# Performance work log

Measured on AMD Instinct MI355X. Metric: run time of the kernel, lower is better.

## Reference

```python
import jax, jax.numpy as jnp
import numpy as np


def _edt_background(gt):
    """Exact Euclidean distance transform of (1 - gt): distance from each pixel
    to the nearest foreground (gt==1) pixel. gt: [H, W] int. Returns [H, W] f32.
    Separable formulation: g(i,j) = 1D distance along row i to nearest fg;
    D(i,j)^2 = min_{i'} ( (i-i')^2 + g(i',j)^2 ), which is the exact 2D EDT.
    """
    H, W = gt.shape
    BIG = jnp.float32(H + W)  # upper bound on any true distance
    fg = gt > 0
    col = jnp.arange(W, dtype=jnp.float32)
    # nearest fg index to the left (running max of fg column index)
    left = jax.lax.cummax(jnp.where(fg, col, -BIG), axis=1)
    d_left = col[None, :] - left
    # nearest fg index to the right: running max of (-col) from the right = -min(col)
    right = jax.lax.cummax(jnp.where(fg, -col, -BIG)[:, ::-1], axis=1)[:, ::-1]
    d_right = (-right) - col[None, :]
    g = jnp.clip(jnp.minimum(d_left, d_right), 0.0, BIG)  # [H, W] 1D row distances
    g2 = g * g
    row = jnp.arange(H, dtype=jnp.float32)
    di2 = (row[:, None] - row[None, :]) ** 2              # [H, H]
    d2 = jnp.min(di2[:, :, None] + g2[None, :, :], axis=1)  # [H, W]
    return jnp.sqrt(d2)


def setup_inputs() -> dict:
    key = jax.random.key(0)
    k1, k2 = jax.random.split(key)
    B, H, W = 16, 384, 384
    logits = jax.random.normal(k1, (B, 1, H, W), dtype=jnp.float32)
    targets = jax.random.randint(k2, (B, 1, H, W), 0, 2).astype(jnp.int32)
    return {"logits": logits, "targets": targets}


def reference(logits, targets):
    probs = jax.nn.sigmoid(logits)            # [B,1,H,W]
    gt = targets[:, 0]                        # [B,H,W] int
    # sequential map over batch keeps the [H,H,W] EDT intermediate per-sample
    dist = jax.lax.map(_edt_background, gt)   # [B,H,W] f32
    tgt_f = gt.astype(jnp.float32)
    per_sample = jnp.mean(jnp.abs(probs[:, 0] - tgt_f) * dist, axis=(1, 2))
    return jnp.mean(per_sample)
```

## Files before the change

### kernel.cpp

```cpp
#include <hip/hip_runtime.h>
#include <math.h>


#define BB 16
#define HH 384
#define WW 384
#define WPR 12
#define WPRP 13
#define SW 8
#define NBLK_PER_IMG (WW / SW)
#define THREADS 256
#define BIGD 768

__global__ __launch_bounds__(THREADS) void pack_kernel(
    const int* __restrict__ gt, unsigned* __restrict__ mask) {
  const int idx = blockIdx.x * THREADS + threadIdx.x;
  const bool fg = gt[idx] != 0;
  const unsigned long long m = __ballot(fg);
  const int lane = threadIdx.x & 63;
  if (lane == 0) mask[idx >> 5] = (unsigned)m;
  else if (lane == 32) mask[idx >> 5] = (unsigned)(m >> 32);
}

__global__ __launch_bounds__(THREADS) void boundary_loss_kernel(
    const float* __restrict__ logits, const int* __restrict__ targets,
    const unsigned* __restrict__ mask, float* __restrict__ out) {
  const int blk = blockIdx.x;
  const int b = blk / NBLK_PER_IMG;
  const int j0 = (blk % NBLK_PER_IMG) * SW;
  const int* __restrict__ gt = targets + b * HH * WW;
  const float* __restrict__ lg = logits + b * HH * WW;
  const unsigned* __restrict__ gm = mask + b * HH * WPR;

  __shared__ unsigned m_s[HH * WPRP];
  __shared__ unsigned short g_s[HH * SW];

  for (int s = threadIdx.x; s < HH * WPR; s += THREADS) {
    const int row = s / WPR;
    const int w = s - row * WPR;
    m_s[row * WPRP + w] = gm[s];
  }
  __syncthreads();

  for (int idx = threadIdx.x; idx < HH * SW; idx += THREADS) {
    const int i = idx >> 3;
    const int jj = idx & (SW - 1);
    const int j = j0 + jj;
    const unsigned* __restrict__ mr = m_s + i * WPRP;
    const int w = j >> 5, bpos = j & 31;
    const unsigned cur = mr[w];
    const unsigned lm = cur & (0xFFFFFFFFu >> (31 - bpos));
    int dl = BIGD;
    if (lm) {
      dl = bpos - (31 - __clz(lm));
    } else {
      for (int ww = w - 1; ww >= 0; --ww) {
        const unsigned x = mr[ww];
        if (x) { dl = j - (ww * 32 + 31 - __clz(x)); break; }
      }
    }
    const unsigned rm = cur & (0xFFFFFFFFu << bpos);
    int dr = BIGD;
    if (rm) {
      dr = (__ffs(rm) - 1) - bpos;
    } else {
      for (int ww = w + 1; ww < WPR; ++ww) {
        const unsigned x = mr[ww];
        if (x) { dr = ww * 32 + (__ffs(x) - 1) - j; break; }
      }
    }
    g_s[idx] = (unsigned short)min(min(dl, dr), BIGD);
  }
  __syncthreads();

  float acc = 0.0f;
  for (int idx = threadIdx.x; idx < HH * SW; idx += THREADS) {
    const int i = idx >> 3;
    const int jj = idx & (SW - 1);
    const int j = j0 + jj;
    const int g = g_s[idx];
    int best = g * g;
    for (int r = 1; r * r < best; ++r) {
      const int im = i - r, ip = i + r;
      if (im >= 0) { const int v = g_s[im * SW + jj]; best = min(best, r * r + v * v); }
      if (ip < HH) { const int v = g_s[ip * SW + jj]; best = min(best, r * r + v * v); }
    }
    const float dist = sqrtf((float)best);
    const float x = lg[i * WW + j];
    const float p = 1.0f / (1.0f + expf(-x));
    const float t = (float)gt[i * WW + j];
    acc += fabsf(p - t) * dist;
  }

  __shared__ float red[THREADS / 64];
  for (int off = 32; off > 0; off >>= 1) acc += __shfl_down(acc, off, 64);
  const int lane = threadIdx.x & 63;
  const int wid = threadIdx.x >> 6;
  if (lane == 0) red[wid] = acc;
  __syncthreads();
  if (threadIdx.x == 0) {
    float s = 0.0f;
    for (int w = 0; w < THREADS / 64; ++w) s += red[w];
    atomicAdd(out, s * (1.0f / (float)(BB * HH * WW)));
  }
}

extern "C" void kernel_launch(void* const* d_in, const int* in_sizes, int n_in,
                              void* d_out, int out_size, void* d_ws, size_t ws_size,
                              hipStream_t stream) {
  const float* logits = (const float*)d_in[0];
  const int* targets = (const int*)d_in[1];
  float* out = (float*)d_out;
  unsigned* mask = (unsigned*)d_ws;

  hipMemsetAsync(d_out, 0, sizeof(float), stream);
  pack_kernel<<<(BB * HH * WW) / THREADS, THREADS, 0, stream>>>(targets, mask);
  boundary_loss_kernel<<<BB * NBLK_PER_IMG, THREADS, 0, stream>>>(logits, targets, mask, out);
}
```

Measured before the change: 89.88 us.

## Drop targets read, vectorize loads, fuse output zeroing into pack kernel

The loss kernel no longer reads targets. Foreground pixels have zero distance, so |p - t|·dist reduces to p·dist everywhere. Mask rows are loaded into shared memory as uint4, and each thread now computes row distances and losses for 4 adjacent columns using ushort4/float4 accesses. The output zeroing moves from a separate memset into the pack kernel, and expf becomes the fast __expf. Together these cut global traffic, instruction count and one launch. In exchange, each thread does more serial work per item and the fast exponential is slightly less accurate.

```diff
diff --git a/kernel.cpp b/kernel.cpp
--- a/kernel.cpp
+++ b/kernel.cpp
@@ -8,88 +8,102 @@
 #define WPR 12
 #define WPRP 13
 #define SW 8
-#define NBLK_PER_IMG (WW / SW)
+#define NBLK (WW / SW)
 #define THREADS 256
 #define BIGD 768
 
 __global__ __launch_bounds__(THREADS) void pack_kernel(
-    const int* __restrict__ gt, unsigned* __restrict__ mask) {
+    const int* __restrict__ gt, unsigned* __restrict__ mask,
+    float* __restrict__ out) {
   const int idx = blockIdx.x * THREADS + threadIdx.x;
   const bool fg = gt[idx] != 0;
   const unsigned long long m = __ballot(fg);
   const int lane = threadIdx.x & 63;
   if (lane == 0) mask[idx >> 5] = (unsigned)m;
   else if (lane == 32) mask[idx >> 5] = (unsigned)(m >> 32);
+  if (idx == 0) out[0] = 0.0f;
 }
 
 __global__ __launch_bounds__(THREADS) void boundary_loss_kernel(
-    const float* __restrict__ logits, const int* __restrict__ targets,
-    const unsigned* __restrict__ mask, float* __restrict__ out) {
+    const float* __restrict__ logits, const unsigned* __restrict__ mask,
+    float* __restrict__ out) {
   const int blk = blockIdx.x;
-  const int b = blk / NBLK_PER_IMG;
-  const int j0 = (blk % NBLK_PER_IMG) * SW;
-  const int* __restrict__ gt = targets + b * HH * WW;
+  const int b = blk / NBLK;
+  const int j0 = (blk % NBLK) * SW;
   const float* __restrict__ lg = logits + b * HH * WW;
-  const unsigned* __restrict__ gm = mask + b * HH * WPR;
 
   __shared__ unsigned m_s[HH * WPRP];
   __shared__ unsigned short g_s[HH * SW];
 
-  for (int s = threadIdx.x; s < HH * WPR; s += THREADS) {
-    const int row = s / WPR;
-    const int w = s - row * WPR;
-    m_s[row * WPRP + w] = gm[s];
+  const uint4* __restrict__ gm4 = (const uint4*)(mask + b * HH * WPR);
+  for (int s = threadIdx.x; s < HH * WPR / 4; s += THREADS) {
+    const uint4 v = gm4[s];
+    const int row = s / 3;
+    const int w0 = (s - row * 3) * 4;
+    unsigned* dst = m_s + row * WPRP + w0;
+    dst[0] = v.x; dst[1] = v.y; dst[2] = v.z; dst[3] = v.w;
   }
   __syncthreads();
 
-  for (int idx = threadIdx.x; idx < HH * SW; idx += THREADS) {
-    const int i = idx >> 3;
-    const int jj = idx & (SW - 1);
+  for (int s = threadIdx.x; s < HH * 2; s += THREADS) {
+    const int i = s >> 1;
+    const int jj = (s & 1) * 4;
     const int j = j0 + jj;
     const unsigned* __restrict__ mr = m_s + i * WPRP;
-    const int w = j >> 5, bpos = j & 31;
+    const int w = j >> 5;
+    const int bpos = j & 31;
     const unsigned cur = mr[w];
-    const unsigned lm = cur & (0xFFFFFFFFu >> (31 - bpos));
-    int dl = BIGD;
-    if (lm) {
-      dl = bpos - (31 - __clz(lm));
-    } else {
+
+    int jL = -0x40000;
+    if ((cur & (0xFFFFFFFFu >> (31 - bpos))) == 0u) {
       for (int ww = w - 1; ww >= 0; --ww) {
         const unsigned x = mr[ww];
-        if (x) { dl = j - (ww * 32 + 31 - __clz(x)); break; }
+        if (x) { jL = ww * 32 + 31 - __clz(x); break; }
       }
     }
-    const unsigned rm = cur & (0xFFFFFFFFu << bpos);
-    int dr = BIGD;
-    if (rm) {
-      dr = (__ffs(rm) - 1) - bpos;
-    } else {
+    int jR = 0x40000;
+    if ((cur & (0xFFFFFFFFu << (bpos + 3))) == 0u) {
       for (int ww = w + 1; ww < WPR; ++ww) {
         const unsigned x = mr[ww];
-        if (x) { dr = ww * 32 + (__ffs(x) - 1) - j; break; }
+        if (x) { jR = ww * 32 + __ffs(x) - 1; break; }
       }
     }
-    g_s[idx] = (unsigned short)min(min(dl, dr), BIGD);
+    unsigned short g4[4];
+#pragma unroll
+    for (int c = 0; c < 4; ++c) {
+      const int bc = bpos + c;
+      const int jc = j + c;
+      const unsigned lm = cur & (0xFFFFFFFFu >> (31 - bc));
+      const unsigned rm = cur & (0xFFFFFFFFu << bc);
+      const int dl = lm ? (bc - (31 - __clz(lm))) : (jc - jL);
+      const int dr = rm ? ((__ffs(rm) - 1) - bc) : (jR - jc);
+      g4[c] = (unsigned short)min(min(dl, dr), BIGD);
+    }
+    ushort4 gv; gv.x = g4[0]; gv.y = g4[1]; gv.z = g4[2]; gv.w = g4[3];
+    *(ushort4*)(g_s + i * SW + jj) = gv;
   }
   __syncthreads();
 
   float acc = 0.0f;
-  for (int idx = threadIdx.x; idx < HH * SW; idx += THREADS) {
-    const int i = idx >> 3;
-    const int jj = idx & (SW - 1);
-    const int j = j0 + jj;
-    const int g = g_s[idx];
-    int best = g * g;
-    for (int r = 1; r * r < best; ++r) {
-      const int im = i - r, ip = i + r;
-      if (im >= 0) { const int v = g_s[im * SW + jj]; best = min(best, r * r + v * v); }
-      if (ip < HH) { const int v = g_s[ip * SW + jj]; best = min(best, r * r + v * v); }
+  for (int s = threadIdx.x; s < HH * 2; s += THREADS) {
+    const int i = s >> 1;
+    const int jj = (s & 1) * 4;
+    const ushort4 gv = *(const ushort4*)(g_s + i * SW + jj);
+    const float4 x4 = *(const float4*)(lg + i * WW + j0 + jj);
+    const int gg[4] = {gv.x, gv.y, gv.z, gv.w};
+    const float xs[4] = {x4.x, x4.y, x4.z, x4.w};
+#pragma unroll
+    for (int c = 0; c < 4; ++c) {
+      int best = gg[c] * gg[c];
+      for (int r = 1; r * r < best; ++r) {
+        const int im = i - r, ip = i + r;
+        if (im >= 0) { const int v = g_s[im * SW + jj + c]; best = min(best, r * r + v * v); }
+        if (ip < HH) { const int v = g_s[ip * SW + jj + c]; best = min(best, r * r + v * v); }
+      }
+      const float dist = sqrtf((float)best);
+      const float p = 1.0f / (1.0f + __expf(-xs[c]));
+      acc += p * dist;
     }
-    const float dist = sqrtf((float)best);
-    const float x = lg[i * WW + j];
-    const float p = 1.0f / (1.0f + expf(-x));
-    const float t = (float)gt[i * WW + j];
-    acc += fabsf(p - t) * dist;
   }
 
   __shared__ float red[THREADS / 64];
@@ -99,9 +113,9 @@
   if (lane == 0) red[wid] = acc;
   __syncthreads();
   if (threadIdx.x == 0) {
-    float s = 0.0f;
-    for (int w = 0; w < THREADS / 64; ++w) s += red[w];
-    atomicAdd(out, s * (1.0f / (float)(BB * HH * WW)));
+    float ssum = 0.0f;
+    for (int w = 0; w < THREADS / 64; ++w) ssum += red[w];
+    atomicAdd(out, ssum * (1.0f / (float)(BB * HH * WW)));
   }
 }
 
@@ -113,7 +127,6 @@
   float* out = (float*)d_out;
   unsigned* mask = (unsigned*)d_ws;
 
-  hipMemsetAsync(d_out, 0, sizeof(float), stream);
-  pack_kernel<<<(BB * HH * WW) / THREADS, THREADS, 0, stream>>>(targets, mask);
-  boundary_loss_kernel<<<BB * NBLK_PER_IMG, THREADS, 0, stream>>>(logits, targets, mask, out);
+  pack_kernel<<<(BB * HH * WW) / THREADS, THREADS, 0, stream>>>(targets, mask, out);
+  boundary_loss_kernel<<<BB * NBLK, THREADS, 0, stream>>>(logits, mask, out);
 }
```

Result: faster. 82.28 us (-8.5%).
